# Kernel optimization log

Hardware: AMD Instinct MI355X
Metric: run time of the kernel (lower is better)

## Reference

```python
import jax, jax.numpy as jnp
import numpy as np

N_NODES = 50000
N_EDGES = 800000
HIDDEN = 128
NUM_RBF = 32
N_GRAPHS = 500
VOCAB = 100


def setup_inputs() -> dict:
    key = jax.random.key(0)
    ks = jax.random.split(key, 16)
    x = jax.random.randint(ks[0], (N_NODES,), 0, VOCAB)
    edge_index = jax.random.randint(ks[1], (2, N_EDGES), 0, N_NODES)
    edge_attr = jax.random.normal(ks[2], (N_EDGES, NUM_RBF), dtype=jnp.float32)
    batch = jnp.sort(jax.random.randint(ks[3], (N_NODES,), 0, N_GRAPHS))
    zdim = 2 * HIDDEN + NUM_RBF
    s = 1.0 / np.sqrt(zdim)
    params = {"emb": jax.random.normal(ks[4], (VOCAB, HIDDEN), dtype=jnp.float32)}
    for l, k0 in zip((1, 2, 3), (5, 8, 11)):
        params[f"Wf{l}"] = jax.random.uniform(ks[k0], (zdim, HIDDEN), minval=-s, maxval=s, dtype=jnp.float32)
        params[f"bf{l}"] = jnp.zeros((HIDDEN,), dtype=jnp.float32)
        params[f"Ws{l}"] = jax.random.uniform(ks[k0 + 1], (zdim, HIDDEN), minval=-s, maxval=s, dtype=jnp.float32)
        params[f"bs{l}"] = jnp.zeros((HIDDEN,), dtype=jnp.float32)
    sl = 1.0 / np.sqrt(HIDDEN)
    params["Wlin"] = jax.random.uniform(ks[14], (HIDDEN, HIDDEN), minval=-sl, maxval=sl, dtype=jnp.float32)
    params["blin"] = jnp.zeros((HIDDEN,), dtype=jnp.float32)
    return {"x": x, "edge_index": edge_index, "edge_attr": edge_attr, "batch": batch, **params}


def _cgconv(h, src, dst, edge_attr, Wf, bf, Ws, bs):
    # z = [x_i || x_j || e_ij]; i = target (dst), j = source (src)
    z = jnp.concatenate([h[dst], h[src], edge_attr], axis=-1)  # [E, 2H+D]
    msg = jax.nn.sigmoid(z @ Wf + bf) * jax.nn.softplus(z @ Ws + bs)  # [E, H]
    agg = jax.ops.segment_sum(msg, dst, num_segments=N_NODES)
    return h + agg


def reference(x, edge_index, edge_attr, batch, emb,
              Wf1, bf1, Ws1, bs1, Wf2, bf2, Ws2, bs2, Wf3, bf3, Ws3, bs3,
              Wlin, blin):
    src, dst = edge_index[0], edge_index[1]
    h = emb[x]  # [N, H]
    h = jax.nn.relu(_cgconv(h, src, dst, edge_attr, Wf1, bf1, Ws1, bs1))
    h = jax.nn.relu(_cgconv(h, src, dst, edge_attr, Wf2, bf2, Ws2, bs2))
    h = jax.nn.relu(_cgconv(h, src, dst, edge_attr, Wf3, bf3, Ws3, bs3))
    sums = jax.ops.segment_sum(h, batch, num_segments=N_GRAPHS)  # [G, H]
    counts = jax.ops.segment_sum(jnp.ones((N_NODES,), h.dtype), batch, num_segments=N_GRAPHS)
    pooled = sums / jnp.maximum(counts, 1.0)[:, None]
    return pooled @ Wlin + blin
```

## Files before the change

### kernel.cpp

```cpp
#include <hip/hip_runtime.h>
#include <hip/hip_bf16.h>
#include <hip/hip_fp16.h>
#include <cstdint>
#include <cstddef>

#define NNODES 50000
#define NEDGES 800000
#define HID 128
#define NRBF 32
#define NGRAPH 500
#define NB_SCAN 196
#define EPB 64
#define NEBLK (NEDGES / EPB)
#define SROW 130

typedef __attribute__((ext_vector_type(8))) short short8;
typedef __attribute__((ext_vector_type(4))) float f32x4;

__device__ inline short f2bf(float x) {
  __hip_bfloat16 b = __float2bfloat16(x);
  return *reinterpret_cast<short*>(&b);
}

__device__ inline unsigned int pk_bf16(float a, float b) {
  unsigned int r;
  asm("v_cvt_pk_bf16_f32 %0, %1, %2" : "=v"(r) : "v"(a), "v"(b));
  return r;
}
__device__ inline unsigned int pk_f16(float a, float b) {
  unsigned int r;
  asm("v_cvt_pkrtz_f16_f32 %0, %1, %2" : "=v"(r) : "v"(a), "v"(b));
  return r;
}
__device__ inline unsigned int pk_add_f16(unsigned int a, unsigned int b) {
  unsigned int r;
  asm("v_pk_add_f16 %0, %1, %2" : "=v"(r) : "v"(a), "v"(b));
  return r;
}
__device__ inline float aexp2(float x) {
  float r;
  asm("v_exp_f32 %0, %1" : "=v"(r) : "v"(x));
  return r;
}
__device__ inline float alog2(float x) {
  float r;
  asm("v_log_f32 %0, %1" : "=v"(r) : "v"(x));
  return r;
}

#define SC_F (-1.4426950408889634f)
#define SC_S (1.4426950408889634f)

__global__ void prep_all(
    const float* __restrict__ Wf0, const float* __restrict__ Ws0,
    const float* __restrict__ bf0, const float* __restrict__ bs0,
    const float* __restrict__ Wf1, const float* __restrict__ Ws1,
    const float* __restrict__ bf1, const float* __restrict__ bs1,
    const float* __restrict__ Wf2, const float* __restrict__ Ws2,
    const float* __restrict__ bf2, const float* __restrict__ bs2,
    unsigned short* __restrict__ WtB3, unsigned short* __restrict__ WnB3,
    float* __restrict__ biasv3) {
  const int l = blockIdx.y;
  const float* Wf = (l == 0) ? Wf0 : ((l == 1) ? Wf1 : Wf2);
  const float* Ws = (l == 0) ? Ws0 : ((l == 1) ? Ws1 : Ws2);
  const float* bf = (l == 0) ? bf0 : ((l == 1) ? bf1 : bf2);
  const float* bs = (l == 0) ? bs0 : ((l == 1) ? bs1 : bs2);
  unsigned short* WtB = WtB3 + l * 8192;
  unsigned short* WnB = WnB3 + l * 65536;
  float* biasv = biasv3 + l * 256;

  int i0 = blockIdx.x * blockDim.x + threadIdx.x;
  if (i0 < 8192) {
    int i = i0;
    int j = i & 7, lane = (i >> 3) & 63, t = i >> 9;
    int q = lane >> 4, n = lane & 15;
    int k = q * 8 + j, c = (t & 7) * 16 + n;
    const float* W = (t < 8) ? Wf : Ws;
    const float sc = (t < 8) ? SC_F : SC_S;
    WtB[i] = (unsigned short)f2bf(W[(size_t)(256 + k) * HID + c] * sc);
  } else if (i0 < 8192 + 65536) {
    int i = i0 - 8192;
    int j = i & 7;
    int lane = (i >> 3) & 63;
    int tk = (i >> 9) & 3;
    int tc = i >> 11;
    int q = lane >> 4, n = lane & 15;
    int k = tk * 32 + q * 8 + j;
    float v;
    int which;
    if (tc < 16) {
      int g = tc >> 1;
      which = tc & 1;
      int c = g * 16 + n;
      const float* W = which ? Ws : Wf;
      v = W[(size_t)k * HID + c];
    } else {
      int g = (tc - 16) >> 1;
      which = (tc - 16) & 1;
      int c = g * 16 + n;
      const float* W = which ? Ws : Wf;
      v = W[(size_t)(128 + k) * HID + c];
    }
    WnB[i] = (unsigned short)f2bf(v * (which ? SC_S : SC_F));
    if (i < 256) {
      int c2 = i >> 1, w2 = i & 1;
      biasv[i] = w2 ? bs[c2] * SC_S : bf[c2] * SC_F;
    }
  }
}

__global__ void deg_hist(const int* __restrict__ dst, int* __restrict__ deg) {
  int e = blockIdx.x * blockDim.x + threadIdx.x;
  if (e < NEDGES) atomicAdd(&deg[dst[e]], 1);
}

__global__ __launch_bounds__(256) void scan_block(const int* __restrict__ deg, int* __restrict__ bsum) {
  __shared__ int s[256];
  int i = blockIdx.x * 256 + threadIdx.x;
  s[threadIdx.x] = (i < NNODES) ? deg[i] : 0;
  __syncthreads();
  for (int off = 128; off > 0; off >>= 1) {
    if (threadIdx.x < off) s[threadIdx.x] += s[threadIdx.x + off];
    __syncthreads();
  }
  if (threadIdx.x == 0) bsum[blockIdx.x] = s[0];
}

__global__ __launch_bounds__(256) void scan_top(const int* __restrict__ bsum,
                                                int* __restrict__ bpre) {
  __shared__ int s[256];
  int t = threadIdx.x;
  int v = (t < NB_SCAN) ? bsum[t] : 0;
  s[t] = v;
  __syncthreads();
  for (int off = 1; off < 256; off <<= 1) {
    int u = (t >= off) ? s[t - off] : 0;
    __syncthreads();
    s[t] += u;
    __syncthreads();
  }
  if (t < NB_SCAN) bpre[t] = s[t] - v;
}

__global__ __launch_bounds__(256) void scan_final(const int* __restrict__ deg,
                                                  const int* __restrict__ bpre,
                                                  int* __restrict__ cursor) {
  __shared__ int s[256];
  int i = blockIdx.x * 256 + threadIdx.x;
  int v = (i < NNODES) ? deg[i] : 0;
  s[threadIdx.x] = v;
  __syncthreads();
  for (int off = 1; off < 256; off <<= 1) {
    int t = (threadIdx.x >= off) ? s[threadIdx.x - off] : 0;
    __syncthreads();
    s[threadIdx.x] += t;
    __syncthreads();
  }
  if (i < NNODES) cursor[i] = bpre[blockIdx.x] + s[threadIdx.x] - v;
}

__global__ void scatter_edges_pack(const int* __restrict__ src, const int* __restrict__ dst,
                                   const float* __restrict__ eattr, int* __restrict__ cursor,
                                   int2* __restrict__ se2, unsigned short* __restrict__ eaB) {
  int e = blockIdx.x * blockDim.x + threadIdx.x;
  if (e >= NEDGES) return;
  int d = dst[e];
  int pos = atomicAdd(&cursor[d], 1);
  se2[pos] = make_int2(src[e], d);
  const float* ep = eattr + (size_t)e * NRBF;
  unsigned short* op = eaB + (size_t)pos * NRBF;
#pragma unroll
  for (int part = 0; part < 4; ++part) {
    const float4 v0 = *(const float4*)&ep[part * 8];
    const float4 v1 = *(const float4*)&ep[part * 8 + 4];
    uint4 o;
    o.x = pk_bf16(v0.x, v0.y);
    o.y = pk_bf16(v0.z, v0.w);
    o.z = pk_bf16(v1.x, v1.y);
    o.w = pk_bf16(v1.z, v1.w);
    *(uint4*)&op[part * 8] = o;
  }
}

__global__ __launch_bounds__(256) void node_mfma(
    const int* __restrict__ x, const float* __restrict__ emb,
    float* __restrict__ h, float* __restrict__ agg,
    const unsigned short* __restrict__ WnB, const float* __restrict__ biasv,
    unsigned int* __restrict__ Pdst, unsigned int* __restrict__ Psrc, int mode, int N) {
  const int tid = threadIdx.x;
  const int wv = tid >> 6;
  const int lane = tid & 63;
  const int q = lane >> 4;
  const int n = lane & 15;
  const int nb = blockIdx.x * 32 + (wv >> 1) * 16;
  const int srcwave = wv & 1;
  const int ctile0 = srcwave * 16;

  const bool valid = (nb + n) < N;
  int anode = nb + n;
  if (anode >= N) anode = N - 1;
  float* hp = h + (size_t)anode * HID;

  short8 a[4];
  if (mode == 0) {
    const float* ep = emb + (size_t)x[anode] * HID;
#pragma unroll
    for (int kt = 0; kt < 4; ++kt) {
      const float4 e0 = *(const float4*)&ep[kt * 32 + q * 8];
      const float4 e1 = *(const float4*)&ep[kt * 32 + q * 8 + 4];
      if (valid && !srcwave) {
        *(float4*)&hp[kt * 32 + q * 8] = e0;
        *(float4*)&hp[kt * 32 + q * 8 + 4] = e1;
      }
      union { short8 s8; unsigned int u32[4]; } au;
      au.u32[0] = pk_bf16(e0.x, e0.y);
      au.u32[1] = pk_bf16(e0.z, e0.w);
      au.u32[2] = pk_bf16(e1.x, e1.y);
      au.u32[3] = pk_bf16(e1.z, e1.w);
      a[kt] = au.s8;
    }
  } else {
    float* ap = agg + (size_t)anode * HID;
    float4 ev[8];
#pragma unroll
    for (int kt = 0; kt < 4; ++kt) {
      float4 e0 = *(const float4*)&hp[kt * 32 + q * 8];
      float4 e1 = *(const float4*)&hp[kt * 32 + q * 8 + 4];
      const float4 g0 = *(const float4*)&ap[kt * 32 + q * 8];
      const float4 g1 = *(const float4*)&ap[kt * 32 + q * 8 + 4];
      e0.x = fmaxf(e0.x + g0.x, 0.f); e0.y = fmaxf(e0.y + g0.y, 0.f);
      e0.z = fmaxf(e0.z + g0.z, 0.f); e0.w = fmaxf(e0.w + g0.w, 0.f);
      e1.x = fmaxf(e1.x + g1.x, 0.f); e1.y = fmaxf(e1.y + g1.y, 0.f);
      e1.z = fmaxf(e1.z + g1.z, 0.f); e1.w = fmaxf(e1.w + g1.w, 0.f);
      ev[2 * kt] = e0;
      ev[2 * kt + 1] = e1;
      union { short8 s8; unsigned int u32[4]; } au;
      au.u32[0] = pk_bf16(e0.x, e0.y);
      au.u32[1] = pk_bf16(e0.z, e0.w);
      au.u32[2] = pk_bf16(e1.x, e1.y);
      au.u32[3] = pk_bf16(e1.z, e1.w);
      a[kt] = au.s8;
    }
    __syncthreads();
    if (valid && !srcwave) {
      const float4 z4 = {0.f, 0.f, 0.f, 0.f};
#pragma unroll
      for (int kt = 0; kt < 4; ++kt) {
        *(float4*)&hp[kt * 32 + q * 8] = ev[2 * kt];
        *(float4*)&hp[kt * 32 + q * 8 + 4] = ev[2 * kt + 1];
        *(float4*)&ap[kt * 32 + q * 8] = z4;
        *(float4*)&ap[kt * 32 + q * 8 + 4] = z4;
      }
    }
  }

  const short8* WnB8 = (const short8*)WnB;
  f32x4 acc[16];
#pragma unroll
  for (int tc = 0; tc < 16; ++tc) acc[tc] = (f32x4){0.f, 0.f, 0.f, 0.f};

#pragma unroll
  for (int tc = 0; tc < 16; ++tc) {
#pragma unroll
    for (int kt = 0; kt < 4; ++kt) {
      short8 b = WnB8[((size_t)((ctile0 + tc) * 4 + kt)) * 64 + lane];
      acc[tc] = __builtin_amdgcn_mfma_f32_16x16x32_bf16(a[kt], b, acc[tc], 0, 0, 0);
    }
  }

  if (!srcwave) {
#pragma unroll
    for (int r = 0; r < 4; ++r) {
      const int node = nb + q * 4 + r;
      if (node < N) {
        unsigned int o[8];
#pragma unroll
        for (int g2 = 0; g2 < 8; ++g2) {
          const int c = g2 * 16 + n;
          o[g2] = pk_f16(acc[2 * g2][r] + biasv[2 * c], acc[2 * g2 + 1][r] + biasv[2 * c + 1]);
        }
        *(uint4*)&Pdst[(size_t)node * 128 + n * 8] = make_uint4(o[0], o[1], o[2], o[3]);
        *(uint4*)&Pdst[(size_t)node * 128 + n * 8 + 4] = make_uint4(o[4], o[5], o[6], o[7]);
      }
    }
  } else {
#pragma unroll
    for (int r = 0; r < 4; ++r) {
      const int node = nb + q * 4 + r;
      if (node < N) {
        unsigned int o[8];
#pragma unroll
        for (int g2 = 0; g2 < 8; ++g2) {
          o[g2] = pk_f16(acc[2 * g2][r], acc[2 * g2 + 1][r]);
        }
        *(uint4*)&Psrc[(size_t)node * 128 + n * 8] = make_uint4(o[0], o[1], o[2], o[3]);
        *(uint4*)&Psrc[(size_t)node * 128 + n * 8 + 4] = make_uint4(o[4], o[5], o[6], o[7]);
      }
    }
  }
}

__global__ __launch_bounds__(256) void edge_mfma(
    const unsigned int* __restrict__ Pdst, const unsigned int* __restrict__ Psrc,
    const unsigned short* __restrict__ eaB, const unsigned short* __restrict__ WtB,
    const int2* __restrict__ se2, float* __restrict__ agg) {
  __shared__ unsigned int fsL[EPB * SROW];
  __shared__ int dstL[EPB];
  __shared__ int grpStart[EPB + 1];
  __shared__ int sndS;

  const int tid = threadIdx.x;
  const int base = blockIdx.x * EPB;
  const int lane = tid & 63;

  if (tid < EPB) {
    int2 sd = se2[base + tid];
    dstL[tid] = sd.y;
    int d = sd.y;
    int dprev = __shfl_up(d, 1);
    int flag = (tid == 0 || dprev != d) ? 1 : 0;
    unsigned long long mask = __ballot(flag);
    unsigned long long below = (lane == 63) ? ~0ull : ((1ull << (lane + 1)) - 1);
    int slot = __popcll(mask & below) - 1;
    if (flag) grpStart[slot] = tid;
    if (tid == 0) {
      int nd = __popcll(mask);
      sndS = nd;
      grpStart[nd] = EPB;
    }
  }

  const int wv = tid >> 6;
  const int q = lane >> 4;
  const int n = lane & 15;
  const int rowb = wv * 16 + q * 4;

  const short8 afrag = *(const short8*)&eaB[(size_t)(base + wv * 16 + n) * 32 + q * 8];

  const unsigned int* pp[4];
#pragma unroll
  for (int r = 0; r < 4; ++r) {
    const int s = se2[base + rowb + r].x;
    pp[r] = Psrc + (size_t)s * 128 + n * 8;
  }

  const short8* WtB8 = (const short8*)WtB;
  const f32x4 zero4 = {0.f, 0.f, 0.f, 0.f};
#pragma unroll
  for (int half = 0; half < 2; ++half) {
    uint4 ps4[4];
#pragma unroll
    for (int r = 0; r < 4; ++r) ps4[r] = *(const uint4*)&pp[r][half * 4];
#pragma unroll
    for (int tt = 0; tt < 4; ++tt) {
      const int t = half * 4 + tt;
      short8 bfr = WtB8[t * 64 + lane];
      short8 bsr = WtB8[(8 + t) * 64 + lane];
      f32x4 cf = __builtin_amdgcn_mfma_f32_16x16x32_bf16(afrag, bfr, zero4, 0, 0, 0);
      f32x4 cs = __builtin_amdgcn_mfma_f32_16x16x32_bf16(afrag, bsr, zero4, 0, 0, 0);
#pragma unroll
      for (int r = 0; r < 4; ++r) {
        const unsigned int psv = (tt == 0) ? ps4[r].x : (tt == 1) ? ps4[r].y
                                : (tt == 2) ? ps4[r].z : ps4[r].w;
        fsL[(rowb + r) * SROW + t * 16 + n] = pk_add_f16(pk_f16(cf[r], cs[r]), psv);
      }
    }
  }
  __syncthreads();

  const int nd = sndS;
  const int l7 = lane & 7, l3 = lane >> 3;
  for (int g = wv; g < nd; g += 4) {
    const int jb = grpStart[g];
    const int je = grpStart[g + 1];
    const int d = __builtin_amdgcn_readfirstlane(dstL[jb]);
    const unsigned int pdx = Pdst[(size_t)d * 128 + 16 * l7 + l3];
    const unsigned int pdy = Pdst[(size_t)d * 128 + 16 * l7 + 8 + l3];
    float acc0 = 0.f, acc1 = 0.f;

    uint2 pk_nx = *(const uint2*)&fsL[jb * SROW + 2 * lane];
    for (int j = jb; j < je; ++j) {
      const uint2 pk = pk_nx;
      int jn = (j + 1 < je) ? (j + 1) : j;
      pk_nx = *(const uint2*)&fsL[jn * SROW + 2 * lane];

      const unsigned int zx = pk_add_f16(pk.x, pdx);
      const unsigned int zy = pk_add_f16(pk.y, pdy);
      const float2 z0 = __half22float2(*reinterpret_cast<const __half2*>(&zx));
      const float2 z1 = __half22float2(*reinterpret_cast<const __half2*>(&zy));
      const float sig0 = __builtin_amdgcn_rcpf(1.f + aexp2(z0.x));
      const float sig1 = __builtin_amdgcn_rcpf(1.f + aexp2(z1.x));
      const float sp0 = fmaxf(z0.y, 0.f) + alog2(1.f + aexp2(fminf(z0.y, -z0.y)));
      const float sp1 = fmaxf(z1.y, 0.f) + alog2(1.f + aexp2(fminf(z1.y, -z1.y)));
      acc0 = fmaf(sig0, sp0, acc0);
      acc1 = fmaf(sig1, sp1, acc1);
    }
    acc0 *= 0.6931471805599453f;
    acc1 *= 0.6931471805599453f;
    float* ap = agg + (size_t)d * HID + 2 * lane;
    if (g == 0 || g == nd - 1) {
      atomicAdd(ap, acc0);
      atomicAdd(ap + 1, acc1);
    } else {
      *(float2*)ap = make_float2(acc0, acc1);
    }
  }
}

__global__ __launch_bounds__(256) void pool_kernel(
    const float* __restrict__ h, const float* __restrict__ agg,
    const int* __restrict__ batch, float* __restrict__ sums, float* __restrict__ counts) {
  __shared__ int gidL[64];
  __shared__ int grpS[65];
  __shared__ int sndP;

  const int tid = threadIdx.x;
  const int lane = tid & 63;
  const int wv = tid >> 6;
  const int nb = blockIdx.x * 64;
  int nvalid = NNODES - nb;
  if (nvalid > 64) nvalid = 64;

  if (tid < 64) {
    int node = nb + tid;
    int g = batch[node < NNODES ? node : NNODES - 1];
    gidL[tid] = g;
    int gprev = __shfl_up(g, 1);
    int flag = (tid < nvalid && (tid == 0 || gprev != g)) ? 1 : 0;
    unsigned long long mask = __ballot(flag);
    int slot = __popcll(mask & ((lane == 63) ? ~0ull : ((1ull << (lane + 1)) - 1))) - 1;
    if (flag) grpS[slot] = tid;
    if (tid == 0) {
      int nd = __popcll(mask);
      sndP = nd;
      grpS[nd] = nvalid;
    }
  }
  __syncthreads();

  const int nd = sndP;
  for (int g = wv; g < nd; g += 4) {
    const int jb = grpS[g];
    const int je = grpS[g + 1];
    const int gid = __builtin_amdgcn_readfirstlane(gidL[jb]);
    float a0 = 0.f, a1 = 0.f;
    for (int j = jb; j < je; ++j) {
      const float2 hv = *(const float2*)&h[(size_t)(nb + j) * HID + 2 * lane];
      const float2 av = *(const float2*)&agg[(size_t)(nb + j) * HID + 2 * lane];
      a0 += fmaxf(hv.x + av.x, 0.f);
      a1 += fmaxf(hv.y + av.y, 0.f);
    }
    float* sp = sums + (size_t)gid * HID + 2 * lane;
    const bool bnd = (g == 0 || g == nd - 1);
    if (bnd) {
      atomicAdd(sp, a0);
      atomicAdd(sp + 1, a1);
    } else {
      *(float2*)sp = make_float2(a0, a1);
    }
    if (lane == 0) {
      if (bnd) atomicAdd(&counts[gid], (float)(je - jb));
      else counts[gid] = (float)(je - jb);
    }
  }
}

__global__ __launch_bounds__(128) void final_kernel(
    const float* __restrict__ sums, const float* __restrict__ counts,
    const float* __restrict__ Wlin, const float* __restrict__ blin,
    float* __restrict__ out) {
  int g = blockIdx.x;
  int c = threadIdx.x;
  __shared__ float pool[HID];
  float cnt = counts[g];
  cnt = cnt > 1.f ? cnt : 1.f;
  pool[c] = sums[(size_t)g * HID + c] / cnt;
  __syncthreads();
  float acc = blin[c];
#pragma unroll 8
  for (int k = 0; k < HID; ++k) acc = fmaf(pool[k], Wlin[k * HID + c], acc);
  out[(size_t)g * HID + c] = acc;
}

extern "C" void kernel_launch(void* const* d_in, const int* in_sizes, int n_in,
                              void* d_out, int out_size, void* d_ws, size_t ws_size,
                              hipStream_t stream) {
  const int* x = (const int*)d_in[0];
  const int* eidx = (const int*)d_in[1];
  const float* eattr = (const float*)d_in[2];
  const int* batch = (const int*)d_in[3];
  const float* emb = (const float*)d_in[4];
  const float* Wf[3] = {(const float*)d_in[5], (const float*)d_in[9], (const float*)d_in[13]};
  const float* bf[3] = {(const float*)d_in[6], (const float*)d_in[10], (const float*)d_in[14]};
  const float* Ws[3] = {(const float*)d_in[7], (const float*)d_in[11], (const float*)d_in[15]};
  const float* bs[3] = {(const float*)d_in[8], (const float*)d_in[12], (const float*)d_in[16]};
  const float* Wlin = (const float*)d_in[17];
  const float* blin = (const float*)d_in[18];
  const int* srcp = eidx;
  const int* dstp = eidx + NEDGES;

  float* wsf = (float*)d_ws;
  float* h = wsf;
  float* PdstF = h + (size_t)NNODES * HID;
  float* agg = PdstF + (size_t)NNODES * 256;
  float* sums = agg + (size_t)NNODES * HID;
  float* counts = sums + (size_t)NGRAPH * HID;
  float* biasv3 = counts + NGRAPH;
  unsigned int* Psrc = (unsigned int*)(biasv3 + 768);
  unsigned short* WtB3 = (unsigned short*)(Psrc + (size_t)NNODES * 128);
  unsigned short* WnB3 = WtB3 + 3 * 8192;
  unsigned short* eaB = WnB3 + 3 * 65536;
  int2* se2 = (int2*)(eaB + (size_t)NEDGES * 32);
  int* deg = (int*)(se2 + NEDGES);
  int* cursor = deg + NNODES;
  int* bsum = cursor + NNODES;
  int* bpre = bsum + NB_SCAN;
  unsigned int* Pdst = (unsigned int*)PdstF;

  dim3 pgrid(288, 3);
  prep_all<<<pgrid, 256, 0, stream>>>(Wf[0], Ws[0], bf[0], bs[0],
                                      Wf[1], Ws[1], bf[1], bs[1],
                                      Wf[2], Ws[2], bf[2], bs[2],
                                      WtB3, WnB3, biasv3);

  hipMemsetAsync(deg, 0, NNODES * sizeof(int), stream);
  deg_hist<<<(NEDGES + 255) / 256, 256, 0, stream>>>(dstp, deg);
  scan_block<<<NB_SCAN, 256, 0, stream>>>(deg, bsum);
  scan_top<<<1, 256, 0, stream>>>(bsum, bpre);
  scan_final<<<NB_SCAN, 256, 0, stream>>>(deg, bpre, cursor);
  scatter_edges_pack<<<(NEDGES + 255) / 256, 256, 0, stream>>>(srcp, dstp, eattr, cursor,
                                                               se2, eaB);

  hipMemsetAsync(agg, 0, (size_t)NNODES * HID * sizeof(float), stream);

  const int nblk_node = (NNODES + 31) / 32;
  for (int l = 0; l < 3; ++l) {
    node_mfma<<<nblk_node, 256, 0, stream>>>(x, emb, h, agg, WnB3 + l * 65536,
                                             biasv3 + l * 256, Pdst, Psrc,
                                             l > 0 ? 1 : 0, NNODES);
    edge_mfma<<<NEBLK, 256, 0, stream>>>(Pdst, Psrc, eaB, WtB3 + l * 8192, se2, agg);
  }

  hipMemsetAsync(sums, 0, (size_t)(NGRAPH * HID + NGRAPH) * sizeof(float), stream);
  pool_kernel<<<(NNODES + 63) / 64, 256, 0, stream>>>(h, agg, batch, sums, counts);
  final_kernel<<<NGRAPH, 128, 0, stream>>>(sums, counts, Wlin, blin, (float*)d_out);
}
```

Baseline: 815.9 us.

## Compute edge activations per edge across all waves before segmented reduction

```diff
diff --git a/kernel.cpp b/kernel.cpp
--- a/kernel.cpp
+++ b/kernel.cpp
@@ -312,6 +312,10 @@
   const int tid = threadIdx.x;
   const int base = blockIdx.x * EPB;
   const int lane = tid & 63;
+  const int wv = tid >> 6;
+  const int q = lane >> 4;
+  const int n = lane & 15;
+  const int rowb = wv * 16 + q * 4;
 
   if (tid < EPB) {
     int2 sd = se2[base + tid];
@@ -330,27 +334,31 @@
     }
   }
 
-  const int wv = tid >> 6;
-  const int q = lane >> 4;
-  const int n = lane & 15;
-  const int rowb = wv * 16 + q * 4;
-
   const short8 afrag = *(const short8*)&eaB[(size_t)(base + wv * 16 + n) * 32 + q * 8];
 
   const unsigned int* pp[4];
+  const unsigned int* dp[4];
 #pragma unroll
   for (int r = 0; r < 4; ++r) {
-    const int s = se2[base + rowb + r].x;
-    pp[r] = Psrc + (size_t)s * 128 + n * 8;
+    const int2 sd = se2[base + rowb + r];
+    pp[r] = Psrc + (size_t)sd.x * 128 + n * 8;
+    dp[r] = Pdst + (size_t)sd.y * 128 + n * 8;
   }
 
   const short8* WtB8 = (const short8*)WtB;
   const f32x4 zero4 = {0.f, 0.f, 0.f, 0.f};
 #pragma unroll
   for (int half = 0; half < 2; ++half) {
-    uint4 ps4[4];
-#pragma unroll
-    for (int r = 0; r < 4; ++r) ps4[r] = *(const uint4*)&pp[r][half * 4];
+    uint4 spd[4];
+#pragma unroll
+    for (int r = 0; r < 4; ++r) {
+      const uint4 ps4 = *(const uint4*)&pp[r][half * 4];
+      const uint4 pd4 = *(const uint4*)&dp[r][half * 4];
+      spd[r].x = pk_add_f16(ps4.x, pd4.x);
+      spd[r].y = pk_add_f16(ps4.y, pd4.y);
+      spd[r].z = pk_add_f16(ps4.z, pd4.z);
+      spd[r].w = pk_add_f16(ps4.w, pd4.w);
+    }
 #pragma unroll
     for (int tt = 0; tt < 4; ++tt) {
       const int t = half * 4 + tt;
@@ -360,49 +368,51 @@
       f32x4 cs = __builtin_amdgcn_mfma_f32_16x16x32_bf16(afrag, bsr, zero4, 0, 0, 0);
 #pragma unroll
       for (int r = 0; r < 4; ++r) {
-        const unsigned int psv = (tt == 0) ? ps4[r].x : (tt == 1) ? ps4[r].y
-                                : (tt == 2) ? ps4[r].z : ps4[r].w;
-        fsL[(rowb + r) * SROW + t * 16 + n] = pk_add_f16(pk_f16(cf[r], cs[r]), psv);
+        const unsigned int sv = (tt == 0) ? spd[r].x : (tt == 1) ? spd[r].y
+                               : (tt == 2) ? spd[r].z : spd[r].w;
+        fsL[(rowb + r) * SROW + t * 16 + n] = pk_add_f16(pk_f16(cf[r], cs[r]), sv);
       }
     }
   }
   __syncthreads();
 
+#pragma unroll 4
+  for (int i = 0; i < 16; ++i) {
+    const int e = wv * 16 + i;
+    const uint2 pk = *(const uint2*)&fsL[e * SROW + 2 * lane];
+    const float2 z0 = __half22float2(*reinterpret_cast<const __half2*>(&pk.x));
+    const float2 z1 = __half22float2(*reinterpret_cast<const __half2*>(&pk.y));
+    const float sig0 = __builtin_amdgcn_rcpf(1.f + aexp2(z0.x));
+    const float sig1 = __builtin_amdgcn_rcpf(1.f + aexp2(z1.x));
+    const float sp0 = fmaxf(z0.y, 0.f) + alog2(1.f + aexp2(fminf(z0.y, -z0.y)));
+    const float sp1 = fmaxf(z1.y, 0.f) + alog2(1.f + aexp2(fminf(z1.y, -z1.y)));
+    fsL[e * SROW + lane] = pk_f16(sig0 * sp0, sig1 * sp1);
+  }
+  __syncthreads();
+
   const int nd = sndS;
-  const int l7 = lane & 7, l3 = lane >> 3;
   for (int g = wv; g < nd; g += 4) {
     const int jb = grpStart[g];
     const int je = grpStart[g + 1];
     const int d = __builtin_amdgcn_readfirstlane(dstL[jb]);
-    const unsigned int pdx = Pdst[(size_t)d * 128 + 16 * l7 + l3];
-    const unsigned int pdy = Pdst[(size_t)d * 128 + 16 * l7 + 8 + l3];
-    float acc0 = 0.f, acc1 = 0.f;
-
-    uint2 pk_nx = *(const uint2*)&fsL[jb * SROW + 2 * lane];
+    float a0 = 0.f, a1 = 0.f;
+    unsigned int av_nx = fsL[jb * SROW + lane];
     for (int j = jb; j < je; ++j) {
-      const uint2 pk = pk_nx;
-      int jn = (j + 1 < je) ? (j + 1) : j;
-      pk_nx = *(const uint2*)&fsL[jn * SROW + 2 * lane];
-
-      const unsigned int zx = pk_add_f16(pk.x, pdx);
-      const unsigned int zy = pk_add_f16(pk.y, pdy);
-      const float2 z0 = __half22float2(*reinterpret_cast<const __half2*>(&zx));
-      const float2 z1 = __half22float2(*reinterpret_cast<const __half2*>(&zy));
-      const float sig0 = __builtin_amdgcn_rcpf(1.f + aexp2(z0.x));
-      const float sig1 = __builtin_amdgcn_rcpf(1.f + aexp2(z1.x));
-      const float sp0 = fmaxf(z0.y, 0.f) + alog2(1.f + aexp2(fminf(z0.y, -z0.y)));
-      const float sp1 = fmaxf(z1.y, 0.f) + alog2(1.f + aexp2(fminf(z1.y, -z1.y)));
-      acc0 = fmaf(sig0, sp0, acc0);
-      acc1 = fmaf(sig1, sp1, acc1);
-    }
-    acc0 *= 0.6931471805599453f;
-    acc1 *= 0.6931471805599453f;
+      const unsigned int av = av_nx;
+      const int jn = (j + 1 < je) ? (j + 1) : j;
+      av_nx = fsL[jn * SROW + lane];
+      const float2 a2 = __half22float2(*reinterpret_cast<const __half2*>(&av));
+      a0 += a2.x;
+      a1 += a2.y;
+    }
+    a0 *= 0.6931471805599453f;
+    a1 *= 0.6931471805599453f;
     float* ap = agg + (size_t)d * HID + 2 * lane;
     if (g == 0 || g == nd - 1) {
-      atomicAdd(ap, acc0);
-      atomicAdd(ap + 1, acc1);
+      atomicAdd(ap, a0);
+      atomicAdd(ap + 1, a1);
     } else {
-      *(float2*)ap = make_float2(acc0, acc1);
+      *(float2*)ap = make_float2(a0, a1);
     }
   }
 }
```

Result: slower. 926.9 us (+13.6%).
